# Optimization experiments

Measured on AMD Instinct MI355X. Metric: run time of the kernel, lower is better.

## Reference

```python
import jax, jax.numpy as jnp
import numpy as np

IN_FEATURES = 4096
OUT_FEATURES = 4096
SHARED_ROWS = 512
BATCH = 4096


def setup_inputs() -> dict:
    key = jax.random.key(0)
    k1, k2, k3 = jax.random.split(key, 3)
    x = jax.random.normal(k1, (BATCH, IN_FEATURES), dtype=jnp.float32)
    shared_weights = jax.random.normal(k2, (SHARED_ROWS, IN_FEATURES), dtype=jnp.float32)
    bias = jax.random.normal(k3, (OUT_FEATURES,), dtype=jnp.float32)
    return {"x": x, "shared_weights": shared_weights, "bias": bias}


def reference(x, shared_weights, bias):
    # Original: W = shared_weights.repeat(out_features // shared_rows, 1)  -> [out, in]
    #           y = x @ W.T + bias
    # Row i of W equals shared_weights[i % shared_rows], so the output columns are a
    # tile of the small GEMM result — compute the small GEMM once and tile (same math,
    # avoids materializing the full [out, in] weight).
    reps = OUT_FEATURES // SHARED_ROWS
    y_small = jnp.einsum("bi,ri->br", x, shared_weights)  # [batch, shared_rows]
    y = jnp.tile(y_small, (1, reps)) + bias  # [batch, out_features]
    return y
```

## Files before the change

kernel.cpp:

```cpp
#include <hip/hip_runtime.h>
#include <hip/hip_bf16.h>


typedef __bf16 bf8 __attribute__((ext_vector_type(8)));
typedef float f4 __attribute__((ext_vector_type(4)));
typedef unsigned int uint;
typedef unsigned short ushort;

constexpr int M = 4096;
constexpr int K = 4096;
constexpr int NS = 512;
constexpr int OUTF = 4096;
constexpr int BM = 128, BN = 128, BK = 64;
constexpr int SPLITS = 4;
constexpr int KSPL = K / SPLITS;
constexpr int NITER = KSPL / BK;
constexpr int MT = M / BM;
constexpr int NT = NS / BN;

#define PERM_HI2(hi, lo) __builtin_amdgcn_perm((hi), (lo), 0x07060302u)
#define WAITCNT_VM8 0xF78
#define WAITCNT_VM0 0xF70

__device__ __forceinline__ void async16(const ushort* g, ushort* l) {
  __builtin_amdgcn_global_load_lds(
      (const __attribute__((address_space(1))) void*)g,
      (__attribute__((address_space(3))) void*)l, 16, 0, 0);
}

__global__ __launch_bounds__(256)
void convert_kernel(const float* __restrict__ x, const float* __restrict__ w,
                    ushort* __restrict__ xb, ushort* __restrict__ wb) {
  const size_t i = (size_t)blockIdx.x * 256 + threadIdx.x;
  constexpr size_t NX = (size_t)M * K / 8;
  const float* src;
  ushort* dst;
  if (i < NX) { src = x + i * 8; dst = xb + i * 8; }
  else        { const size_t j = i - NX; src = w + j * 8; dst = wb + j * 8; }
  const uint4 a = *reinterpret_cast<const uint4*>(src);
  const uint4 b = *reinterpret_cast<const uint4*>(src + 4);
  uint4 o;
  o.x = PERM_HI2(a.y, a.x); o.y = PERM_HI2(a.w, a.z);
  o.z = PERM_HI2(b.y, b.x); o.w = PERM_HI2(b.w, b.z);
  *reinterpret_cast<uint4*>(dst) = o;
}

__global__ __launch_bounds__(256, 2)
void gemm_kernel(const ushort* __restrict__ xb, const ushort* __restrict__ wb,
                 float* __restrict__ out) {
  __shared__ __align__(16) ushort As[2][BM * BK];
  __shared__ __align__(16) ushort Bs[2][BN * BK];

  const int b   = blockIdx.x;
  const int low = b & 7, h = b >> 3;
  const int mt  = (h >> 4) * 8 + low;
  const int sp  = (h >> 2) & 3;
  const int nt  = h & 3;

  const int tid  = threadIdx.x;
  const int wv   = tid >> 6;
  const int lane = tid & 63;
  const int lr   = lane & 15;
  const int lq   = lane >> 4;

  int goff[4], lloc[4];
#pragma unroll
  for (int j = 0; j < 4; ++j) {
    const int c = (wv * 4 + j) * 64 + lane;
    const int r = c >> 3;
    const int g = (c & 7) ^ (r & 7);
    goff[j] = r * K + g * 8;
    lloc[j] = c * 8;
  }

  const ushort* xT = xb + (size_t)(mt * BM) * K + sp * KSPL;
  const ushort* wT = wb + (size_t)(nt * BN) * K + sp * KSPL;

  auto issue = [&](int tile, int stg) {
    const int ko = tile * BK;
#pragma unroll
    for (int j = 0; j < 4; ++j) {
      async16(xT + ko + goff[j], &As[stg][lloc[j]]);
      async16(wT + ko + goff[j], &Bs[stg][lloc[j]]);
    }
  };

  const int wm = (wv & 1) * 64;
  const int wn = (wv >> 1) * 64;

  f4 acc[4][4] = {};

  issue(0, 0);
  issue(1, 1);

  int st = 0;
  for (int kk = 0; kk < NITER; ++kk) {
    if (kk + 1 < NITER) __builtin_amdgcn_s_waitcnt(WAITCNT_VM8);
    else                __builtin_amdgcn_s_waitcnt(WAITCNT_VM0);
    __builtin_amdgcn_s_barrier();
    asm volatile("" ::: "memory");

    const ushort* aT = As[st];
    const ushort* bT = Bs[st];
#pragma unroll
    for (int t = 0; t < 2; ++t) {
      const int sc = ((t * 4 + lq) ^ (lr & 7)) * 8;
      bf8 af[4], bfv[4];
#pragma unroll
      for (int mf = 0; mf < 4; ++mf)
        af[mf] = *reinterpret_cast<const bf8*>(&aT[(wm + mf * 16 + lr) * BK + sc]);
#pragma unroll
      for (int nf = 0; nf < 4; ++nf)
        bfv[nf] = *reinterpret_cast<const bf8*>(&bT[(wn + nf * 16 + lr) * BK + sc]);
#pragma unroll
      for (int mf = 0; mf < 4; ++mf)
#pragma unroll
        for (int nf = 0; nf < 4; ++nf)
          acc[mf][nf] = __builtin_amdgcn_mfma_f32_16x16x32_bf16(af[mf], bfv[nf], acc[mf][nf], 0, 0, 0);
    }
    asm volatile("" ::: "memory");
    __builtin_amdgcn_s_barrier();
    asm volatile("" ::: "memory");
    if (kk + 2 < NITER) issue(kk + 2, st);
    st ^= 1;
  }

  float* pb = out + (size_t)(mt * BM) * OUTF + sp * NS + nt * BN;
#pragma unroll
  for (int mf = 0; mf < 4; ++mf)
#pragma unroll
    for (int nf = 0; nf < 4; ++nf)
#pragma unroll
      for (int r = 0; r < 4; ++r)
        pb[(size_t)(wm + mf * 16 + lq * 4 + r) * OUTF + wn + nf * 16 + lr] =
            acc[mf][nf][r];
}

__global__ __launch_bounds__(256)
void combine_kernel(const float* __restrict__ bias, float* __restrict__ out) {
  const int idx = blockIdx.x * 256 + threadIdx.x;
  const int row = idx >> 7;
  const int c4  = idx & 127;
  float* orow = out + (size_t)row * OUTF;
  float4 s;
  {
    const float4 p0 = *reinterpret_cast<const float4*>(orow + 0 * NS + c4 * 4);
    const float4 p1 = *reinterpret_cast<const float4*>(orow + 1 * NS + c4 * 4);
    const float4 p2 = *reinterpret_cast<const float4*>(orow + 2 * NS + c4 * 4);
    const float4 p3 = *reinterpret_cast<const float4*>(orow + 3 * NS + c4 * 4);
    s.x = (p0.x + p1.x) + (p2.x + p3.x);
    s.y = (p0.y + p1.y) + (p2.y + p3.y);
    s.z = (p0.z + p1.z) + (p2.z + p3.z);
    s.w = (p0.w + p1.w) + (p2.w + p3.w);
  }
  const float4* bias4 = reinterpret_cast<const float4*>(bias);
#pragma unroll
  for (int rep = 0; rep < 8; ++rep) {
    const float4 bb = bias4[rep * 128 + c4];
    float4 o;
    o.x = s.x + bb.x; o.y = s.y + bb.y;
    o.z = s.z + bb.z; o.w = s.w + bb.w;
    *reinterpret_cast<float4*>(orow + rep * NS + c4 * 4) = o;
  }
}

extern "C" void kernel_launch(void* const* d_in, const int* in_sizes, int n_in,
                              void* d_out, int out_size, void* d_ws, size_t ws_size,
                              hipStream_t stream) {
  (void)in_sizes; (void)n_in; (void)out_size; (void)ws_size;
  const float* x    = (const float*)d_in[0];
  const float* w    = (const float*)d_in[1];
  const float* bias = (const float*)d_in[2];
  float* out = (float*)d_out;

  ushort* xb = (ushort*)d_ws;
  ushort* wb = (ushort*)d_ws + (size_t)M * K;

  constexpr int conv_blocks = (int)(((size_t)M * K / 8 + (size_t)NS * K / 8) / 256);
  convert_kernel<<<dim3(conv_blocks), dim3(256), 0, stream>>>(x, w, xb, wb);
  gemm_kernel<<<dim3(MT * NT * SPLITS), dim3(256), 0, stream>>>(xb, wb, out);
  combine_kernel<<<dim3(M * (NS / 4) / 256), dim3(256), 0, stream>>>(bias, out);
}
```

Measured before the change: 150.8 us.

## Fuse x fp32-to-bf16 conversion into GEMM LDS path with triple buffering

The separate pass that converts x to bf16 is removed. The GEMM now streams fp32 x tiles straight into LDS and truncates them to bf16 on the fly when forming MFMA operands, so x is no longer written to and re-read from a workspace. BK drops to 32 and the LDS ring grows to three stages, which removes the second barrier per iteration by issuing the prefetch right after the wait. In exchange, each stage moves twice the bytes for A, and each K-step does extra permute work and makes more barrier round trips.

```diff
diff --git a/kernel.cpp b/kernel.cpp
--- a/kernel.cpp
+++ b/kernel.cpp
@@ -11,7 +11,7 @@
 constexpr int K = 4096;
 constexpr int NS = 512;
 constexpr int OUTF = 4096;
-constexpr int BM = 128, BN = 128, BK = 64;
+constexpr int BM = 128, BN = 128, BK = 32;
 constexpr int SPLITS = 4;
 constexpr int KSPL = K / SPLITS;
 constexpr int NITER = KSPL / BK;
@@ -19,24 +19,20 @@
 constexpr int NT = NS / BN;
 
 #define PERM_HI2(hi, lo) __builtin_amdgcn_perm((hi), (lo), 0x07060302u)
-#define WAITCNT_VM8 0xF78
+#define WAITCNT_VM6 0xF76
 #define WAITCNT_VM0 0xF70
 
-__device__ __forceinline__ void async16(const ushort* g, ushort* l) {
+__device__ __forceinline__ void async16(const void* g, void* l) {
   __builtin_amdgcn_global_load_lds(
       (const __attribute__((address_space(1))) void*)g,
       (__attribute__((address_space(3))) void*)l, 16, 0, 0);
 }
 
 __global__ __launch_bounds__(256)
-void convert_kernel(const float* __restrict__ x, const float* __restrict__ w,
-                    ushort* __restrict__ xb, ushort* __restrict__ wb) {
+void convert_w(const float* __restrict__ w, ushort* __restrict__ wb) {
   const size_t i = (size_t)blockIdx.x * 256 + threadIdx.x;
-  constexpr size_t NX = (size_t)M * K / 8;
-  const float* src;
-  ushort* dst;
-  if (i < NX) { src = x + i * 8; dst = xb + i * 8; }
-  else        { const size_t j = i - NX; src = w + j * 8; dst = wb + j * 8; }
+  const float* src = w + i * 8;
+  ushort* dst = wb + i * 8;
   const uint4 a = *reinterpret_cast<const uint4*>(src);
   const uint4 b = *reinterpret_cast<const uint4*>(src + 4);
   uint4 o;
@@ -46,10 +42,10 @@
 }
 
 __global__ __launch_bounds__(256, 2)
-void gemm_kernel(const ushort* __restrict__ xb, const ushort* __restrict__ wb,
+void gemm_kernel(const float* __restrict__ x, const ushort* __restrict__ wb,
                  float* __restrict__ out) {
-  __shared__ __align__(16) ushort As[2][BM * BK];
-  __shared__ __align__(16) ushort Bs[2][BN * BK];
+  __shared__ __align__(16) float  As[3][BM * BK];
+  __shared__ __align__(16) ushort Bs[3][BN * BK];
 
   const int b   = blockIdx.x;
   const int low = b & 7, h = b >> 3;
@@ -63,26 +59,34 @@
   const int lr   = lane & 15;
   const int lq   = lane >> 4;
 
-  int goff[4], lloc[4];
+  int goffA[4], llocA[4];
 #pragma unroll
   for (int j = 0; j < 4; ++j) {
     const int c = (wv * 4 + j) * 64 + lane;
     const int r = c >> 3;
     const int g = (c & 7) ^ (r & 7);
-    goff[j] = r * K + g * 8;
-    lloc[j] = c * 8;
+    goffA[j] = r * K + g * 4;
+    llocA[j] = c * 4;
+  }
+  int goffB[2], llocB[2];
+#pragma unroll
+  for (int j = 0; j < 2; ++j) {
+    const int c = (wv * 2 + j) * 64 + lane;
+    const int r = c >> 2;
+    const int g = (c & 3) ^ (r & 3);
+    goffB[j] = r * K + g * 8;
+    llocB[j] = c * 8;
   }
 
-  const ushort* xT = xb + (size_t)(mt * BM) * K + sp * KSPL;
+  const float*  xT = x  + (size_t)(mt * BM) * K + sp * KSPL;
   const ushort* wT = wb + (size_t)(nt * BN) * K + sp * KSPL;
 
   auto issue = [&](int tile, int stg) {
     const int ko = tile * BK;
 #pragma unroll
-    for (int j = 0; j < 4; ++j) {
-      async16(xT + ko + goff[j], &As[stg][lloc[j]]);
-      async16(wT + ko + goff[j], &Bs[stg][lloc[j]]);
-    }
+    for (int j = 0; j < 4; ++j) async16(xT + ko + goffA[j], &As[stg][llocA[j]]);
+#pragma unroll
+    for (int j = 0; j < 2; ++j) async16(wT + ko + goffB[j], &Bs[stg][llocB[j]]);
   };
 
   const int wm = (wv & 1) * 64;
@@ -95,34 +99,46 @@
 
   int st = 0;
   for (int kk = 0; kk < NITER; ++kk) {
-    if (kk + 1 < NITER) __builtin_amdgcn_s_waitcnt(WAITCNT_VM8);
+    if (kk + 1 < NITER) __builtin_amdgcn_s_waitcnt(WAITCNT_VM6);
     else                __builtin_amdgcn_s_waitcnt(WAITCNT_VM0);
     __builtin_amdgcn_s_barrier();
     asm volatile("" ::: "memory");
 
-    const ushort* aT = As[st];
+    if (kk + 2 < NITER) {
+      int s2 = st + 2; if (s2 >= 3) s2 -= 3;
+      issue(kk + 2, s2);
+    }
+
+    const float*  aT = As[st];
     const ushort* bT = Bs[st];
+    bf8 af[4], bfv[4];
 #pragma unroll
-    for (int t = 0; t < 2; ++t) {
-      const int sc = ((t * 4 + lq) ^ (lr & 7)) * 8;
-      bf8 af[4], bfv[4];
+    for (int mf = 0; mf < 4; ++mf) {
+      const int row = wm + mf * 16 + lr;
+      const int ca  = (2 * lq) ^ (lr & 7);
+      const f4 a0 = *reinterpret_cast<const f4*>(&aT[row * BK + ca * 4]);
+      const f4 a1 = *reinterpret_cast<const f4*>(&aT[row * BK + (ca ^ 1) * 4]);
+      const uint* u0 = reinterpret_cast<const uint*>(&a0);
+      const uint* u1 = reinterpret_cast<const uint*>(&a1);
+      uint4 p;
+      p.x = PERM_HI2(u0[1], u0[0]); p.y = PERM_HI2(u0[3], u0[2]);
+      p.z = PERM_HI2(u1[1], u1[0]); p.w = PERM_HI2(u1[3], u1[2]);
+      af[mf] = __builtin_bit_cast(bf8, p);
+    }
 #pragma unroll
-      for (int mf = 0; mf < 4; ++mf)
-        af[mf] = *reinterpret_cast<const bf8*>(&aT[(wm + mf * 16 + lr) * BK + sc]);
+    for (int nf = 0; nf < 4; ++nf) {
+      const int rowb = wn + nf * 16 + lr;
+      const int sb   = lq ^ (lr & 3);
+      bfv[nf] = *reinterpret_cast<const bf8*>(&bT[rowb * BK + sb * 8]);
+    }
+#pragma unroll
+    for (int mf = 0; mf < 4; ++mf)
 #pragma unroll
       for (int nf = 0; nf < 4; ++nf)
-        bfv[nf] = *reinterpret_cast<const bf8*>(&bT[(wn + nf * 16 + lr) * BK + sc]);
-#pragma unroll
-      for (int mf = 0; mf < 4; ++mf)
-#pragma unroll
-        for (int nf = 0; nf < 4; ++nf)
-          acc[mf][nf] = __builtin_amdgcn_mfma_f32_16x16x32_bf16(af[mf], bfv[nf], acc[mf][nf], 0, 0, 0);
-    }
+        acc[mf][nf] = __builtin_amdgcn_mfma_f32_16x16x32_bf16(af[mf], bfv[nf], acc[mf][nf], 0, 0, 0);
     asm volatile("" ::: "memory");
-    __builtin_amdgcn_s_barrier();
-    asm volatile("" ::: "memory");
-    if (kk + 2 < NITER) issue(kk + 2, st);
-    st ^= 1;
+
+    if (++st >= 3) st = 0;
   }
 
   float* pb = out + (size_t)(mt * BM) * OUTF + sp * NS + nt * BN;
@@ -173,11 +189,10 @@
   const float* bias = (const float*)d_in[2];
   float* out = (float*)d_out;
 
-  ushort* xb = (ushort*)d_ws;
-  ushort* wb = (ushort*)d_ws + (size_t)M * K;
+  ushort* wb = (ushort*)d_ws;
 
-  constexpr int conv_blocks = (int)(((size_t)M * K / 8 + (size_t)NS * K / 8) / 256);
-  convert_kernel<<<dim3(conv_blocks), dim3(256), 0, stream>>>(x, w, xb, wb);
-  gemm_kernel<<<dim3(MT * NT * SPLITS), dim3(256), 0, stream>>>(xb, wb, out);
+  constexpr int convw_blocks = (int)((size_t)NS * K / 8 / 256);
+  convert_w<<<dim3(convw_blocks), dim3(256), 0, stream>>>(w, wb);
+  gemm_kernel<<<dim3(MT * NT * SPLITS), dim3(256), 0, stream>>>(x, wb, out);
   combine_kernel<<<dim3(M * (NS / 4) / 256), dim3(256), 0, stream>>>(bias, out);
 }
```

Result: slower. 178.7 us (+18.5%).

## Use 128x256 tiles, 8-way split-K, triple-buffered LDS, XCD-aware combine

Applied to the files above, without the earlier changes.

The GEMM tile becomes 128x256 with BK=32 and split-K goes from 4 to 8, so the grid stays the same size while each block does more MFMAs per loaded A byte. LDS moves to three stages, which lets the next prefetch be issued right after the barrier and removes the second barrier per iteration. The combine kernel now sums 8 partials and maps blocks to rows by XCD so reads stay local to the chiplet's L2. The costs are more accumulator registers (128 floats per thread), twice as many partial sums written and read, and a shorter K loop per block.

```diff
diff --git a/kernel.cpp b/kernel.cpp
--- a/kernel.cpp
+++ b/kernel.cpp
@@ -11,15 +11,15 @@
 constexpr int K = 4096;
 constexpr int NS = 512;
 constexpr int OUTF = 4096;
-constexpr int BM = 128, BN = 128, BK = 64;
-constexpr int SPLITS = 4;
+constexpr int BM = 128, BN = 256, BK = 32;
+constexpr int SPLITS = 8;
 constexpr int KSPL = K / SPLITS;
 constexpr int NITER = KSPL / BK;
 constexpr int MT = M / BM;
 constexpr int NT = NS / BN;
 
 #define PERM_HI2(hi, lo) __builtin_amdgcn_perm((hi), (lo), 0x07060302u)
-#define WAITCNT_VM8 0xF78
+#define WAITCNT_VM6 0xF76
 #define WAITCNT_VM0 0xF70
 
 __device__ __forceinline__ void async16(const ushort* g, ushort* l) {
@@ -48,14 +48,14 @@
 __global__ __launch_bounds__(256, 2)
 void gemm_kernel(const ushort* __restrict__ xb, const ushort* __restrict__ wb,
                  float* __restrict__ out) {
-  __shared__ __align__(16) ushort As[2][BM * BK];
-  __shared__ __align__(16) ushort Bs[2][BN * BK];
+  __shared__ __align__(16) ushort As[3][BM * BK];
+  __shared__ __align__(16) ushort Bs[3][BN * BK];
 
   const int b   = blockIdx.x;
   const int low = b & 7, h = b >> 3;
   const int mt  = (h >> 4) * 8 + low;
-  const int sp  = (h >> 2) & 3;
-  const int nt  = h & 3;
+  const int sp  = (h >> 1) & 7;
+  const int nt  = h & 1;
 
   const int tid  = threadIdx.x;
   const int wv   = tid >> 6;
@@ -63,14 +63,23 @@
   const int lr   = lane & 15;
   const int lq   = lane >> 4;
 
-  int goff[4], lloc[4];
+  int goffA[2], llocA[2];
+#pragma unroll
+  for (int j = 0; j < 2; ++j) {
+    const int c = (wv * 2 + j) * 64 + lane;
+    const int r = c >> 2;
+    const int g = (c & 3) ^ (r & 3);
+    goffA[j] = r * K + g * 8;
+    llocA[j] = c * 8;
+  }
+  int goffB[4], llocB[4];
 #pragma unroll
   for (int j = 0; j < 4; ++j) {
     const int c = (wv * 4 + j) * 64 + lane;
-    const int r = c >> 3;
-    const int g = (c & 7) ^ (r & 7);
-    goff[j] = r * K + g * 8;
-    lloc[j] = c * 8;
+    const int r = c >> 2;
+    const int g = (c & 3) ^ (r & 3);
+    goffB[j] = r * K + g * 8;
+    llocB[j] = c * 8;
   }
 
   const ushort* xT = xb + (size_t)(mt * BM) * K + sp * KSPL;
@@ -79,57 +88,56 @@
   auto issue = [&](int tile, int stg) {
     const int ko = tile * BK;
 #pragma unroll
-    for (int j = 0; j < 4; ++j) {
-      async16(xT + ko + goff[j], &As[stg][lloc[j]]);
-      async16(wT + ko + goff[j], &Bs[stg][lloc[j]]);
-    }
+    for (int j = 0; j < 2; ++j) async16(xT + ko + goffA[j], &As[stg][llocA[j]]);
+#pragma unroll
+    for (int j = 0; j < 4; ++j) async16(wT + ko + goffB[j], &Bs[stg][llocB[j]]);
   };
 
   const int wm = (wv & 1) * 64;
-  const int wn = (wv >> 1) * 64;
+  const int wn = (wv >> 1) * 128;
+  const int coff = (lq ^ (lr & 3)) * 8;
 
-  f4 acc[4][4] = {};
+  f4 acc[4][8] = {};
 
   issue(0, 0);
   issue(1, 1);
 
   int st = 0;
   for (int kk = 0; kk < NITER; ++kk) {
-    if (kk + 1 < NITER) __builtin_amdgcn_s_waitcnt(WAITCNT_VM8);
+    if (kk + 1 < NITER) __builtin_amdgcn_s_waitcnt(WAITCNT_VM6);
     else                __builtin_amdgcn_s_waitcnt(WAITCNT_VM0);
     __builtin_amdgcn_s_barrier();
     asm volatile("" ::: "memory");
 
+    if (kk + 2 < NITER) {
+      int s2 = st + 2; if (s2 >= 3) s2 -= 3;
+      issue(kk + 2, s2);
+    }
+
     const ushort* aT = As[st];
     const ushort* bT = Bs[st];
+    bf8 af[4], bfv[8];
 #pragma unroll
-    for (int t = 0; t < 2; ++t) {
-      const int sc = ((t * 4 + lq) ^ (lr & 7)) * 8;
-      bf8 af[4], bfv[4];
+    for (int mf = 0; mf < 4; ++mf)
+      af[mf] = *reinterpret_cast<const bf8*>(&aT[(wm + mf * 16 + lr) * BK + coff]);
 #pragma unroll
-      for (int mf = 0; mf < 4; ++mf)
-        af[mf] = *reinterpret_cast<const bf8*>(&aT[(wm + mf * 16 + lr) * BK + sc]);
+    for (int nf = 0; nf < 8; ++nf)
+      bfv[nf] = *reinterpret_cast<const bf8*>(&bT[(wn + nf * 16 + lr) * BK + coff]);
 #pragma unroll
-      for (int nf = 0; nf < 4; ++nf)
-        bfv[nf] = *reinterpret_cast<const bf8*>(&bT[(wn + nf * 16 + lr) * BK + sc]);
+    for (int mf = 0; mf < 4; ++mf)
 #pragma unroll
-      for (int mf = 0; mf < 4; ++mf)
-#pragma unroll
-        for (int nf = 0; nf < 4; ++nf)
-          acc[mf][nf] = __builtin_amdgcn_mfma_f32_16x16x32_bf16(af[mf], bfv[nf], acc[mf][nf], 0, 0, 0);
-    }
+      for (int nf = 0; nf < 8; ++nf)
+        acc[mf][nf] = __builtin_amdgcn_mfma_f32_16x16x32_bf16(af[mf], bfv[nf], acc[mf][nf], 0, 0, 0);
     asm volatile("" ::: "memory");
-    __builtin_amdgcn_s_barrier();
-    asm volatile("" ::: "memory");
-    if (kk + 2 < NITER) issue(kk + 2, st);
-    st ^= 1;
+
+    if (++st >= 3) st = 0;
   }
 
   float* pb = out + (size_t)(mt * BM) * OUTF + sp * NS + nt * BN;
 #pragma unroll
   for (int mf = 0; mf < 4; ++mf)
 #pragma unroll
-    for (int nf = 0; nf < 4; ++nf)
+    for (int nf = 0; nf < 8; ++nf)
 #pragma unroll
       for (int r = 0; r < 4; ++r)
         pb[(size_t)(wm + mf * 16 + lq * 4 + r) * OUTF + wn + nf * 16 + lr] =
@@ -138,9 +146,13 @@
 
 __global__ __launch_bounds__(256)
 void combine_kernel(const float* __restrict__ bias, float* __restrict__ out) {
-  const int idx = blockIdx.x * 256 + threadIdx.x;
-  const int row = idx >> 7;
-  const int c4  = idx & 127;
+  const int xcd = blockIdx.x & 7;
+  const int q   = blockIdx.x >> 3;
+  const int idx = q * 256 + threadIdx.x;
+  const int lrow = idx >> 7;
+  const int c4   = idx & 127;
+  const int mt   = xcd + (lrow >> 7) * 8;
+  const int row  = mt * 128 + (lrow & 127);
   float* orow = out + (size_t)row * OUTF;
   float4 s;
   {
@@ -148,10 +160,14 @@
     const float4 p1 = *reinterpret_cast<const float4*>(orow + 1 * NS + c4 * 4);
     const float4 p2 = *reinterpret_cast<const float4*>(orow + 2 * NS + c4 * 4);
     const float4 p3 = *reinterpret_cast<const float4*>(orow + 3 * NS + c4 * 4);
-    s.x = (p0.x + p1.x) + (p2.x + p3.x);
-    s.y = (p0.y + p1.y) + (p2.y + p3.y);
-    s.z = (p0.z + p1.z) + (p2.z + p3.z);
-    s.w = (p0.w + p1.w) + (p2.w + p3.w);
+    const float4 p4 = *reinterpret_cast<const float4*>(orow + 4 * NS + c4 * 4);
+    const float4 p5 = *reinterpret_cast<const float4*>(orow + 5 * NS + c4 * 4);
+    const float4 p6 = *reinterpret_cast<const float4*>(orow + 6 * NS + c4 * 4);
+    const float4 p7 = *reinterpret_cast<const float4*>(orow + 7 * NS + c4 * 4);
+    s.x = ((p0.x + p1.x) + (p2.x + p3.x)) + ((p4.x + p5.x) + (p6.x + p7.x));
+    s.y = ((p0.y + p1.y) + (p2.y + p3.y)) + ((p4.y + p5.y) + (p6.y + p7.y));
+    s.z = ((p0.z + p1.z) + (p2.z + p3.z)) + ((p4.z + p5.z) + (p6.z + p7.z));
+    s.w = ((p0.w + p1.w) + (p2.w + p3.w)) + ((p4.w + p5.w) + (p6.w + p7.w));
   }
   const float4* bias4 = reinterpret_cast<const float4*>(bias);
 #pragma unroll
```

Measured after the change: 166.0 us. 10.1% more time.

## Fuse split-K reduction and bias tiling into GEMM via atomic tickets

Applied to the files above, without the earlier changes.

Drops the separate combine kernel. Each split-K block now writes its partial tile and increments a per-tile atomic ticket. The last-arriving block sums the other partials from global memory, adds bias and writes all eight replicated column tiles. This removes a kernel launch and a full pass over the partial buffer. In exchange it adds an atomic and fences, and the reduction work lands on a quarter of the blocks at the tail of the GEMM.

```diff
diff --git a/kernel.cpp b/kernel.cpp
--- a/kernel.cpp
+++ b/kernel.cpp
@@ -17,6 +17,7 @@
 constexpr int NITER = KSPL / BK;
 constexpr int MT = M / BM;
 constexpr int NT = NS / BN;
+constexpr int NTILES = MT * NT;
 
 #define PERM_HI2(hi, lo) __builtin_amdgcn_perm((hi), (lo), 0x07060302u)
 #define WAITCNT_VM8 0xF78
@@ -30,7 +31,9 @@
 
 __global__ __launch_bounds__(256)
 void convert_kernel(const float* __restrict__ x, const float* __restrict__ w,
-                    ushort* __restrict__ xb, ushort* __restrict__ wb) {
+                    ushort* __restrict__ xb, ushort* __restrict__ wb,
+                    uint* __restrict__ tickets) {
+  if (blockIdx.x == 0 && threadIdx.x < NTILES) tickets[threadIdx.x] = 0u;
   const size_t i = (size_t)blockIdx.x * 256 + threadIdx.x;
   constexpr size_t NX = (size_t)M * K / 8;
   const float* src;
@@ -47,7 +50,8 @@
 
 __global__ __launch_bounds__(256, 2)
 void gemm_kernel(const ushort* __restrict__ xb, const ushort* __restrict__ wb,
-                 float* __restrict__ out) {
+                 const float* __restrict__ bias, float* __restrict__ out,
+                 uint* __restrict__ tickets) {
   __shared__ __align__(16) ushort As[2][BM * BK];
   __shared__ __align__(16) ushort Bs[2][BN * BK];
 
@@ -125,43 +129,54 @@
     st ^= 1;
   }
 
-  float* pb = out + (size_t)(mt * BM) * OUTF + sp * NS + nt * BN;
+  const int colb = nt * BN + wn;
+  float* pb = out + (size_t)(mt * BM) * OUTF + sp * NS + colb;
 #pragma unroll
   for (int mf = 0; mf < 4; ++mf)
 #pragma unroll
     for (int nf = 0; nf < 4; ++nf)
 #pragma unroll
       for (int r = 0; r < 4; ++r)
-        pb[(size_t)(wm + mf * 16 + lq * 4 + r) * OUTF + wn + nf * 16 + lr] =
+        pb[(size_t)(wm + mf * 16 + lq * 4 + r) * OUTF + nf * 16 + lr] =
             acc[mf][nf][r];
-}
 
-__global__ __launch_bounds__(256)
-void combine_kernel(const float* __restrict__ bias, float* __restrict__ out) {
-  const int idx = blockIdx.x * 256 + threadIdx.x;
-  const int row = idx >> 7;
-  const int c4  = idx & 127;
-  float* orow = out + (size_t)row * OUTF;
-  float4 s;
-  {
-    const float4 p0 = *reinterpret_cast<const float4*>(orow + 0 * NS + c4 * 4);
-    const float4 p1 = *reinterpret_cast<const float4*>(orow + 1 * NS + c4 * 4);
-    const float4 p2 = *reinterpret_cast<const float4*>(orow + 2 * NS + c4 * 4);
-    const float4 p3 = *reinterpret_cast<const float4*>(orow + 3 * NS + c4 * 4);
-    s.x = (p0.x + p1.x) + (p2.x + p3.x);
-    s.y = (p0.y + p1.y) + (p2.y + p3.y);
-    s.z = (p0.z + p1.z) + (p2.z + p3.z);
-    s.w = (p0.w + p1.w) + (p2.w + p3.w);
+  __syncthreads();
+  uint* s_oldp = reinterpret_cast<uint*>(&As[0][0]);
+  if (tid == 0) {
+    __threadfence();
+    *s_oldp = __hip_atomic_fetch_add(&tickets[mt * NT + nt], 1u,
+                                     __ATOMIC_ACQ_REL, __HIP_MEMORY_SCOPE_AGENT);
   }
-  const float4* bias4 = reinterpret_cast<const float4*>(bias);
+  __syncthreads();
+  if (*s_oldp != SPLITS - 1) return;
+  if (tid == 0) __threadfence();
+  __syncthreads();
+
+  float bv[8][4];
 #pragma unroll
-  for (int rep = 0; rep < 8; ++rep) {
-    const float4 bb = bias4[rep * 128 + c4];
-    float4 o;
-    o.x = s.x + bb.x; o.y = s.y + bb.y;
-    o.z = s.z + bb.z; o.w = s.w + bb.w;
-    *reinterpret_cast<float4*>(orow + rep * NS + c4 * 4) = o;
-  }
+  for (int rep = 0; rep < 8; ++rep)
+#pragma unroll
+    for (int nf = 0; nf < 4; ++nf)
+      bv[rep][nf] = bias[rep * NS + colb + nf * 16 + lr];
+
+  float* ob = out + (size_t)(mt * BM) * OUTF + colb;
+#pragma unroll
+  for (int mf = 0; mf < 4; ++mf)
+#pragma unroll
+    for (int r = 0; r < 4; ++r) {
+      const size_t rowoff = (size_t)(wm + mf * 16 + lq * 4 + r) * OUTF;
+#pragma unroll
+      for (int nf = 0; nf < 4; ++nf) {
+        const int co = nf * 16 + lr;
+        float s = acc[mf][nf][r];
+#pragma unroll
+        for (int p = 0; p < SPLITS; ++p)
+          if (p != sp) s += ob[rowoff + p * NS + co];
+#pragma unroll
+        for (int rep = 0; rep < 8; ++rep)
+          ob[rowoff + rep * NS + co] = s + bv[rep][nf];
+      }
+    }
 }
 
 extern "C" void kernel_launch(void* const* d_in, const int* in_sizes, int n_in,
@@ -175,9 +190,9 @@
 
   ushort* xb = (ushort*)d_ws;
   ushort* wb = (ushort*)d_ws + (size_t)M * K;
+  uint* tickets = (uint*)(wb + (size_t)NS * K);
 
   constexpr int conv_blocks = (int)(((size_t)M * K / 8 + (size_t)NS * K / 8) / 256);
-  convert_kernel<<<dim3(conv_blocks), dim3(256), 0, stream>>>(x, w, xb, wb);
-  gemm_kernel<<<dim3(MT * NT * SPLITS), dim3(256), 0, stream>>>(xb, wb, out);
-  combine_kernel<<<dim3(M * (NS / 4) / 256), dim3(256), 0, stream>>>(bias, out);
+  convert_kernel<<<dim3(conv_blocks), dim3(256), 0, stream>>>(x, w, xb, wb, tickets);
+  gemm_kernel<<<dim3(MT * NT * SPLITS), dim3(256), 0, stream>>>(xb, wb, bias, out, tickets);
 }
```

New measurement: 238.0 us. 57.8% more time.
